# Kernel optimization log

Measured on AMD Instinct MI355X. Metric: run time of the kernel, lower is better.

The kernel has to match this reference:

```python
import jax, jax.numpy as jnp
import numpy as np

# Layer configuration (from init_kwargs)
T = 32
TSEQ = jnp.linspace(1.0 / T, 1.0, T, dtype=jnp.float32)  # tseq grid
N_HOM_DIMS = 2      # dimensions = [0, 1]
KMAX = 4            # KK = [0,1,2,3] -> top-4 landscapes

B, N, P = 128, 256 * 256, 4096  # batch, grid cells, persistence pairs


def setup_inputs() -> dict:
    key = jax.random.key(0)
    k1, k2, k3, k4 = jax.random.split(key, 4)
    fun_value = jax.random.uniform(k1, (B, N), dtype=jnp.float32)
    birth_idx = jax.random.randint(k2, (B, P), 0, N, dtype=jnp.int32)
    death_idx = jax.random.randint(k3, (B, P), 0, N, dtype=jnp.int32)
    pair_dim = jax.random.randint(k4, (B, P), 0, N_HOM_DIMS, dtype=jnp.int32)
    return {"fun_value": fun_value, "birth_idx": birth_idx,
            "death_idx": death_idx, "pair_dim": pair_dim}


def reference(fun_value, birth_idx, death_idx, pair_dim):
    # Gather birth/death filtration values of each persistence pair
    # (this is fun_value[locationBirth] / fun_value[locationDeath]).
    b = jnp.take_along_axis(fun_value, birth_idx, axis=-1)   # [B, P]
    d = jnp.take_along_axis(fun_value, death_idx, axis=-1)   # [B, P]
    # Tent functions: fab[b, t, p] = max(min(tseq[t] - birth_p, death_p - tseq[t]), 0)
    fab = jnp.maximum(
        jnp.minimum(TSEQ[None, :, None] - b[:, None, :],
                    d[:, None, :] - TSEQ[None, :, None]),
        0.0)                                                  # [B, T, P]
    # Restrict pairs to each homology dimension; out-of-dim pairs become the
    # zero padding the original code uses in its fab buffer.
    dims = jnp.arange(N_HOM_DIMS, dtype=pair_dim.dtype)
    in_dim = pair_dim[:, None, None, :] == dims[None, :, None, None]  # [B, D, 1, P]
    fab_d = jnp.where(in_dim, fab[:, None, :, :], 0.0)        # [B, D, T, P]
    # Landscape = top-KMAX values over pairs (== -sort(-fab)[..., KK]).
    land, _ = jax.lax.top_k(fab_d, KMAX)                      # [B, D, T, KMAX]
    return land
```

## Files before the change

### kernel.cpp

```cpp
#include <hip/hip_runtime.h>

#define B_ 128
#define N_ 65536
#define P_ 4096
#define T_ 32
#define D_ 2
#define K_ 4
#define S_ 8
#define PPB 512

#define INS(v0, v1, v2, v3, val)                                  \
    {                                                             \
        float _x = fminf(v0, val); v0 = fmaxf(v0, val);           \
        float _y = fminf(v1, _x);  v1 = fmaxf(v1, _x);            \
        float _z = fminf(v2, _y);  v2 = fmaxf(v2, _y);            \
        v3 = fmaxf(v3, _z);                                       \
    }

__global__ __launch_bounds__(256) void fused_scan(
        const float* __restrict__ fun,
        const int* __restrict__ bidx,
        const int* __restrict__ didx,
        const int* __restrict__ pdim,
        float* __restrict__ partial) {
    __shared__ float2 bdS[PPB + 8];
    __shared__ int    cntS[8];
    __shared__ float  mrg[4][64][4];

    int bid   = blockIdx.x;
    int xcd   = bid & 7;
    int seq   = bid >> 3;
    int batch = xcd * 16 + (seq & 15);
    int slice = seq >> 4;

    int tid  = threadIdx.x;
    int lane = tid & 63;
    int wave = tid >> 6;
    int base = batch * P_ + slice * PPB;

    const float* f = fun + (size_t)batch * N_;
    int p0 = base + tid, p1 = base + 256 + tid;
    int pd0 = pdim[p0], pd1 = pdim[p1];
    float b0 = f[bidx[p0]], d0 = f[didx[p0]];
    float b1 = f[bidx[p1]], d1 = f[didx[p1]];

    unsigned long long bal0 = __ballot(pd0 == 0);
    unsigned long long bal1 = __ballot(pd1 == 0);
    if (lane == 0) {
        cntS[wave * 2]     = __popcll(bal0);
        cntS[wave * 2 + 1] = __popcll(bal1);
    }
    __syncthreads();

    int s0 = wave * 2, s1 = s0 + 1;
    int pre0_s0 = 0, pre1_s0 = 0, pre0_s1 = 0, pre1_s1 = 0, n0tot = 0;
    #pragma unroll
    for (int s = 0; s < 8; ++s) {
        int cs = cntS[s];
        if (s < s0) { pre0_s0 += cs; pre1_s0 += 64 - cs; }
        if (s < s1) { pre0_s1 += cs; pre1_s1 += 64 - cs; }
        n0tot += cs;
    }
    int n1tot = PPB - n0tot;
    int A   = (n0tot + 1) & ~1;
    int n1p = (n1tot + 1) & ~1;

    unsigned long long lmask = (1ull << lane) - 1ull;
    int r0 = __popcll(bal0 & lmask);
    int r1 = __popcll(bal1 & lmask);
    int dst0 = (pd0 == 0) ? (pre0_s0 + r0) : (A + pre1_s0 + (lane - r0));
    int dst1 = (pd1 == 0) ? (pre0_s1 + r1) : (A + pre1_s1 + (lane - r1));
    bdS[dst0] = make_float2(b0, d0);
    bdS[dst1] = make_float2(b1, d1);
    if (tid == 0 && (n0tot & 1)) bdS[n0tot]     = make_float2(4.f, -4.f);
    if (tid == 1 && (n1tot & 1)) bdS[A + n1tot] = make_float2(4.f, -4.f);
    __syncthreads();

    int half = lane >> 5;
    int t    = lane & 31;
    float tf = (float)(t + 1) * 0.03125f;

    float a0 = 0.f, a1 = 0.f, a2 = 0.f, a3 = 0.f;
    float c0 = 0.f, c1 = 0.f, c2 = 0.f, c3 = 0.f;

    #pragma unroll 4
    for (int j = wave * 2; j < A; j += 8) {
        float2 p = bdS[j + half];
        float val = fminf(tf - p.x, p.y - tf);
        INS(a0, a1, a2, a3, val);
    }
    #pragma unroll 4
    for (int j = A + wave * 2; j < A + n1p; j += 8) {
        float2 p = bdS[j + half];
        float val = fminf(tf - p.x, p.y - tf);
        INS(c0, c1, c2, c3, val);
    }

    float u0 = (half == 0) ? a0 : c0, w0 = (half == 0) ? c0 : a0;
    float u1 = (half == 0) ? a1 : c1, w1 = (half == 0) ? c1 : a1;
    float u2 = (half == 0) ? a2 : c2, w2 = (half == 0) ? c2 : a2;
    float u3 = (half == 0) ? a3 : c3, w3 = (half == 0) ? c3 : a3;
    float q;
    q = __shfl_xor(w0, 32); INS(u0, u1, u2, u3, q);
    q = __shfl_xor(w1, 32); INS(u0, u1, u2, u3, q);
    q = __shfl_xor(w2, 32); INS(u0, u1, u2, u3, q);
    q = __shfl_xor(w3, 32); INS(u0, u1, u2, u3, q);

    mrg[wave][lane][0] = u0;
    mrg[wave][lane][1] = u1;
    mrg[wave][lane][2] = u2;
    mrg[wave][lane][3] = u3;
    __syncthreads();

    if (wave == 0) {
        float v0 = 0.f, v1 = 0.f, v2 = 0.f, v3 = 0.f;
        #pragma unroll
        for (int w = 0; w < 4; ++w) {
            #pragma unroll
            for (int k = 0; k < 4; ++k) {
                float val = mrg[w][lane][k];
                INS(v0, v1, v2, v3, val);
            }
        }
        float* dst = partial + (((size_t)batch * S_ + slice) * 64 + lane) * 4;
        dst[0] = v0; dst[1] = v1; dst[2] = v2; dst[3] = v3;
    }
}

__global__ __launch_bounds__(256) void final_merge(
        const float* __restrict__ partial,
        float* __restrict__ out) {
    int tid   = blockIdx.x * 256 + threadIdx.x;
    int batch = tid >> 6;
    int combo = tid & 63;
    float v0 = 0.f, v1 = 0.f, v2 = 0.f, v3 = 0.f;
    for (int s = 0; s < S_; ++s) {
        const float* src = partial + (((size_t)batch * S_ + s) * 64 + combo) * 4;
        #pragma unroll
        for (int k = 0; k < 4; ++k) {
            float val = src[k];
            INS(v0, v1, v2, v3, val);
        }
    }
    float* dst = out + (size_t)tid * 4;
    dst[0] = v0; dst[1] = v1; dst[2] = v2; dst[3] = v3;
}

extern "C" void kernel_launch(void* const* d_in, const int* in_sizes, int n_in,
                              void* d_out, int out_size, void* d_ws, size_t ws_size,
                              hipStream_t stream) {
    const float* fun  = (const float*)d_in[0];
    const int*   bidx = (const int*)d_in[1];
    const int*   didx = (const int*)d_in[2];
    const int*   pdim = (const int*)d_in[3];
    float* out = (float*)d_out;

    float* partial = (float*)d_ws;

    fused_scan<<<B_ * S_, 256, 0, stream>>>(fun, bidx, didx, pdim, partial);
    final_merge<<<(B_ * 64) / 256, 256, 0, stream>>>(partial, out);
}
```

Before: 90.27 us.

## Filter empty persistence pairs before compaction and vectorize LDS and index loads

Pairs whose death is not above their birth can never give a positive tent value, so they are now dropped during the per-dimension compaction. This shrinks the scan lists, which are padded to multiples of four. The scan loop reads two pairs per float4 LDS load. The index and dimension arrays are read as int2, and the partial and output stores use float4. The gain depends on how many pairs the data lets it discard, and the extra ballots and compaction add overhead.

```diff
diff --git a/kernel.cpp b/kernel.cpp
--- a/kernel.cpp
+++ b/kernel.cpp
@@ -23,9 +23,10 @@
         const int* __restrict__ didx,
         const int* __restrict__ pdim,
         float* __restrict__ partial) {
-    __shared__ float2 bdS[PPB + 8];
-    __shared__ int    cntS[8];
-    __shared__ float  mrg[4][64][4];
+    __shared__ __align__(16) float2 bdS[PPB + 8];
+    __shared__ int cnt0S[8];
+    __shared__ int cnt1S[8];
+    __shared__ float mrg[4][64][4];
 
     int bid   = blockIdx.x;
     int xcd   = bid & 7;
@@ -39,41 +40,46 @@
     int base = batch * P_ + slice * PPB;
 
     const float* f = fun + (size_t)batch * N_;
-    int p0 = base + tid, p1 = base + 256 + tid;
-    int pd0 = pdim[p0], pd1 = pdim[p1];
-    float b0 = f[bidx[p0]], d0 = f[didx[p0]];
-    float b1 = f[bidx[p1]], d1 = f[didx[p1]];
+    int2 bi = ((const int2*)(bidx + base))[tid];
+    int2 di = ((const int2*)(didx + base))[tid];
+    int2 pd = ((const int2*)(pdim + base))[tid];
+    float be = f[bi.x], de = f[di.x];
+    float bo = f[bi.y], dd = f[di.y];
 
-    unsigned long long bal0 = __ballot(pd0 == 0);
-    unsigned long long bal1 = __ballot(pd1 == 0);
+    bool k0e = (pd.x == 0) && (de > be);
+    bool k1e = (pd.x == 1) && (de > be);
+    bool k0o = (pd.y == 0) && (dd > bo);
+    bool k1o = (pd.y == 1) && (dd > bo);
+
+    unsigned long long b0e = __ballot(k0e), b1e = __ballot(k1e);
+    unsigned long long b0o = __ballot(k0o), b1o = __ballot(k1o);
     if (lane == 0) {
-        cntS[wave * 2]     = __popcll(bal0);
-        cntS[wave * 2 + 1] = __popcll(bal1);
+        cnt0S[wave * 2]     = __popcll(b0e);
+        cnt0S[wave * 2 + 1] = __popcll(b0o);
+        cnt1S[wave * 2]     = __popcll(b1e);
+        cnt1S[wave * 2 + 1] = __popcll(b1o);
     }
     __syncthreads();
 
-    int s0 = wave * 2, s1 = s0 + 1;
-    int pre0_s0 = 0, pre1_s0 = 0, pre0_s1 = 0, pre1_s1 = 0, n0tot = 0;
+    int ce = wave * 2, co = ce + 1;
+    int pre0e = 0, pre0o = 0, pre1e = 0, pre1o = 0, tot0 = 0, tot1 = 0;
     #pragma unroll
-    for (int s = 0; s < 8; ++s) {
-        int cs = cntS[s];
-        if (s < s0) { pre0_s0 += cs; pre1_s0 += 64 - cs; }
-        if (s < s1) { pre0_s1 += cs; pre1_s1 += 64 - cs; }
-        n0tot += cs;
+    for (int c = 0; c < 8; ++c) {
+        int c0 = cnt0S[c], c1 = cnt1S[c];
+        if (c < ce) { pre0e += c0; pre1e += c1; }
+        if (c < co) { pre0o += c0; pre1o += c1; }
+        tot0 += c0; tot1 += c1;
     }
-    int n1tot = PPB - n0tot;
-    int A   = (n0tot + 1) & ~1;
-    int n1p = (n1tot + 1) & ~1;
+    int A  = (tot0 + 3) & ~3;
+    int L1 = (tot1 + 3) & ~3;
 
-    unsigned long long lmask = (1ull << lane) - 1ull;
-    int r0 = __popcll(bal0 & lmask);
-    int r1 = __popcll(bal1 & lmask);
-    int dst0 = (pd0 == 0) ? (pre0_s0 + r0) : (A + pre1_s0 + (lane - r0));
-    int dst1 = (pd1 == 0) ? (pre0_s1 + r1) : (A + pre1_s1 + (lane - r1));
-    bdS[dst0] = make_float2(b0, d0);
-    bdS[dst1] = make_float2(b1, d1);
-    if (tid == 0 && (n0tot & 1)) bdS[n0tot]     = make_float2(4.f, -4.f);
-    if (tid == 1 && (n1tot & 1)) bdS[A + n1tot] = make_float2(4.f, -4.f);
+    unsigned long long lm = (1ull << lane) - 1ull;
+    if (k0e) bdS[pre0e + __popcll(b0e & lm)]     = make_float2(be, de);
+    if (k1e) bdS[A + pre1e + __popcll(b1e & lm)] = make_float2(be, de);
+    if (k0o) bdS[pre0o + __popcll(b0o & lm)]     = make_float2(bo, dd);
+    if (k1o) bdS[A + pre1o + __popcll(b1o & lm)] = make_float2(bo, dd);
+    if (tid < A - tot0)                    bdS[tot0 + tid]           = make_float2(4.f, -4.f);
+    if (tid >= 4 && tid - 4 < L1 - tot1)   bdS[A + tot1 + (tid - 4)] = make_float2(4.f, -4.f);
     __syncthreads();
 
     int half = lane >> 5;
@@ -83,17 +89,22 @@
     float a0 = 0.f, a1 = 0.f, a2 = 0.f, a3 = 0.f;
     float c0 = 0.f, c1 = 0.f, c2 = 0.f, c3 = 0.f;
 
-    #pragma unroll 4
-    for (int j = wave * 2; j < A; j += 8) {
-        float2 p = bdS[j + half];
-        float val = fminf(tf - p.x, p.y - tf);
-        INS(a0, a1, a2, a3, val);
+    const float2* bd0 = bdS + 2 * half;
+    #pragma unroll 2
+    for (int j = wave * 4; j < A; j += 16) {
+        float4 q = *(const float4*)(bd0 + j);
+        float v0 = fminf(tf - q.x, q.y - tf);
+        float v1 = fminf(tf - q.z, q.w - tf);
+        INS(a0, a1, a2, a3, v0);
+        INS(a0, a1, a2, a3, v1);
     }
-    #pragma unroll 4
-    for (int j = A + wave * 2; j < A + n1p; j += 8) {
-        float2 p = bdS[j + half];
-        float val = fminf(tf - p.x, p.y - tf);
-        INS(c0, c1, c2, c3, val);
+    #pragma unroll 2
+    for (int j = wave * 4; j < L1; j += 16) {
+        float4 q = *(const float4*)(bd0 + A + j);
+        float v0 = fminf(tf - q.x, q.y - tf);
+        float v1 = fminf(tf - q.z, q.w - tf);
+        INS(c0, c1, c2, c3, v0);
+        INS(c0, c1, c2, c3, v1);
     }
 
     float u0 = (half == 0) ? a0 : c0, w0 = (half == 0) ? c0 : a0;
@@ -122,8 +133,8 @@
                 INS(v0, v1, v2, v3, val);
             }
         }
-        float* dst = partial + (((size_t)batch * S_ + slice) * 64 + lane) * 4;
-        dst[0] = v0; dst[1] = v1; dst[2] = v2; dst[3] = v3;
+        ((float4*)partial)[((size_t)batch * S_ + slice) * 64 + lane] =
+            make_float4(v0, v1, v2, v3);
     }
 }
 
@@ -133,17 +144,17 @@
     int tid   = blockIdx.x * 256 + threadIdx.x;
     int batch = tid >> 6;
     int combo = tid & 63;
+    const float4* src = (const float4*)partial + (size_t)batch * S_ * 64 + combo;
     float v0 = 0.f, v1 = 0.f, v2 = 0.f, v3 = 0.f;
+    #pragma unroll
     for (int s = 0; s < S_; ++s) {
-        const float* src = partial + (((size_t)batch * S_ + s) * 64 + combo) * 4;
-        #pragma unroll
-        for (int k = 0; k < 4; ++k) {
-            float val = src[k];
-            INS(v0, v1, v2, v3, val);
-        }
+        float4 p = src[(size_t)s * 64];
+        INS(v0, v1, v2, v3, p.x);
+        INS(v0, v1, v2, v3, p.y);
+        INS(v0, v1, v2, v3, p.z);
+        INS(v0, v1, v2, v3, p.w);
     }
-    float* dst = out + (size_t)tid * 4;
-    dst[0] = v0; dst[1] = v1; dst[2] = v2; dst[3] = v3;
+    ((float4*)out)[tid] = make_float4(v0, v1, v2, v3);
 }
 
 extern "C" void kernel_launch(void* const* d_in, const int* in_sizes, int n_in,
```

After: 87.73 us (median of 2 runs). -2.8%, faster.
